# Kernel optimization log

Hardware: AMD Instinct MI355X
Metric: run time of the kernel (lower is better)

## Reference

```python
import jax, jax.numpy as jnp
import numpy as np

N = 100000   # nodes
E = 1000000  # edges
IN = 100     # input feature dim
H = 4        # heads
D = 32       # hidden per head (H*D = 128)
C = 47       # classes
EPS = 1e-5
SLOPE = 0.2  # DGL GATv2 leaky_relu negative slope


def setup_inputs() -> dict:
    key = jax.random.key(0)
    ks = jax.random.split(key, 32)
    lin = lambda k, i, o: (jax.random.normal(k, (i, o), jnp.float32) / np.float32(np.sqrt(i)))
    inp = {}
    inp['x'] = jax.random.normal(ks[0], (N, IN), jnp.float32)
    inp['src'] = jax.random.randint(ks[1], (E,), 0, N, jnp.int32)
    inp['dst'] = jnp.sort(jax.random.randint(ks[2], (E,), 0, N, jnp.int32))
    # layer 0: IN -> H*D, Linear residual (IN != H*D)
    inp['Wsrc0'] = lin(ks[3], IN, H * D); inp['bsrc0'] = jnp.zeros(H * D, jnp.float32)
    inp['Wdst0'] = lin(ks[4], IN, H * D); inp['bdst0'] = jnp.zeros(H * D, jnp.float32)
    inp['attn0'] = lin(ks[5], H, D)
    inp['Wres0'] = lin(ks[6], IN, H * D); inp['bres0'] = jnp.zeros(H * D, jnp.float32)
    # layer 1: H*D -> H*D, Identity residual (128 == 128)
    inp['Wsrc1'] = lin(ks[7], H * D, H * D); inp['bsrc1'] = jnp.zeros(H * D, jnp.float32)
    inp['Wdst1'] = lin(ks[8], H * D, H * D); inp['bdst1'] = jnp.zeros(H * D, jnp.float32)
    inp['attn1'] = lin(ks[9], H, D)
    # layer 2: H*D -> H*C, Linear residual (128 != 188)
    inp['Wsrc2'] = lin(ks[10], H * D, H * C); inp['bsrc2'] = jnp.zeros(H * C, jnp.float32)
    inp['Wdst2'] = lin(ks[11], H * D, H * C); inp['bdst2'] = jnp.zeros(H * C, jnp.float32)
    inp['attn2'] = lin(ks[12], H, C)
    inp['Wres2'] = lin(ks[13], H * D, H * C); inp['bres2'] = jnp.zeros(H * C, jnp.float32)
    # BatchNorm1d params (training-mode batch stats)
    inp['g0'] = jnp.ones(H * D, jnp.float32); inp['be0'] = jnp.zeros(H * D, jnp.float32)
    inp['g1'] = jnp.ones(H * D, jnp.float32); inp['be1'] = jnp.zeros(H * D, jnp.float32)
    return inp


def _gatv2(h, src, dst, Ws, bs, Wd, bd, attn, resval):
    """One GATv2Conv on a full block (src feats == dst feats == h)."""
    Hh, Dd = attn.shape
    fs = (h @ Ws + bs).reshape(-1, Hh, Dd)   # [N,H,D] src projection
    fd = (h @ Wd + bd).reshape(-1, Hh, Dd)   # [N,H,D] dst projection
    e = jax.nn.leaky_relu(fs[src] + fd[dst], SLOPE)         # [E,H,D]
    logits = jnp.einsum('ehd,hd->eh', e, attn)              # [E,H]
    m = jax.ops.segment_max(logits, dst, num_segments=N)    # per-dst max
    ex = jnp.exp(logits - m[dst])
    s = jax.ops.segment_sum(ex, dst, num_segments=N)
    alpha = ex / s[dst]                                      # edge softmax
    out = jax.ops.segment_sum(alpha[:, :, None] * fs[src], dst, num_segments=N)
    return out + resval                                      # [N,H,D]


def _bn(x, g, b):
    mu = x.mean(0)
    v = x.var(0)  # biased, as torch BN training mode
    return g * (x - mu) / jnp.sqrt(v + EPS) + b


def reference(x, src, dst,
              Wsrc0, bsrc0, Wdst0, bdst0, attn0, Wres0, bres0,
              Wsrc1, bsrc1, Wdst1, bdst1, attn1,
              Wsrc2, bsrc2, Wdst2, bdst2, attn2, Wres2, bres2,
              g0, be0, g1, be1):
    # layer 0: conv(+relu activation) -> flatten -> BN -> relu (dropout = eval identity)
    res0 = (x @ Wres0 + bres0).reshape(N, H, D)
    h = jax.nn.relu(_gatv2(x, src, dst, Wsrc0, bsrc0, Wdst0, bdst0, attn0, res0))
    h = jax.nn.relu(_bn(h.reshape(N, H * D), g0, be0))
    # layer 1: Identity residual
    res1 = h.reshape(N, H, D)
    h = jax.nn.relu(_gatv2(h, src, dst, Wsrc1, bsrc1, Wdst1, bdst1, attn1, res1))
    h = jax.nn.relu(_bn(h.reshape(N, H * D), g1, be1))
    # layer 2: no activation; mean over heads; log_softmax
    res2 = (h @ Wres2 + bres2).reshape(N, H, C)
    h = _gatv2(h, src, dst, Wsrc2, bsrc2, Wdst2, bdst2, attn2, res2)
    h = h.mean(1)                                # [N,C]
    return jax.nn.log_softmax(h, axis=-1)
```

## Files before the change

### kernel.cpp

```cpp
#include <hip/hip_runtime.h>
#include <hip/hip_bf16.h>

#define Nn 100000
#define Ee 1000000
#define INF_ 100
#define Hh 4
#define Dd 32
#define HD 128
#define Cc 47
#define HC 188
#define HCP 192
#define EPSV 1e-5f
#define SLOPE 0.2f

typedef __hip_bfloat16 bf16;
typedef __attribute__((ext_vector_type(8))) short short8;
typedef __attribute__((ext_vector_type(4))) float f32x4;

__device__ __forceinline__ float tof(bf16 v) { return __bfloat162float(v); }
__device__ __forceinline__ float b2f(unsigned short u) {
    return __uint_as_float((unsigned)u << 16);
}
__device__ __forceinline__ float ldb(const bf16* p) {
    return b2f(*(const unsigned short*)p);
}
__device__ __forceinline__ unsigned short f2u(float v) {
    bf16 t = __float2bfloat16(v);
    return *(unsigned short*)&t;
}

__global__ void detect_dtype(const unsigned* __restrict__ x, int* __restrict__ flag) {
    if (blockIdx.x == 0 && threadIdx.x == 0) {
        int good = 0;
        for (int i = 0; i < 256; ++i) {
            unsigned lo = x[i] & 0xFFFFu;
            float v = __uint_as_float(lo << 16);
            float a = fabsf(v);
            if (a > 1e-4f && a < 10.f) good++;
        }
        *flag = (good >= 128) ? 1 : 0;
    }
}

__device__ __forceinline__ float ld_any(const void* p, int i, int isbf) {
    return isbf ? tof(((const bf16*)p)[i]) : ((const float*)p)[i];
}

__global__ void cvt_x(const void* __restrict__ in, bf16* __restrict__ out,
                      const int* __restrict__ flag) {
    int i = blockIdx.x * blockDim.x + threadIdx.x;
    if (i >= Nn * 128) return;
    int row = i >> 7, col = i & 127;
    float v = (col < INF_) ? ld_any(in, row * INF_ + col, *flag) : 0.f;
    out[i] = __float2bfloat16(v);
}

#define NSP 15
struct CvtTab { const void* src[NSP]; int off[NSP + 1]; };

__global__ void cvt_params(CvtTab t, bf16* __restrict__ out, int total,
                           const int* __restrict__ flag) {
    int i = blockIdx.x * blockDim.x + threadIdx.x;
    if (i >= total) return;
    int isbf = *flag;
    int seg = 0;
    while (i >= t.off[seg + 1]) seg++;
    out[i] = __float2bfloat16(ld_any(t.src[seg], i - t.off[seg], isbf));
}

#define WROWS 1280
struct PrepTab { const void* src[8]; int row0[8]; int K[8]; int M[8]; int MP[8]; };

__global__ void prep_all(PrepTab t, bf16* __restrict__ wtb, const int* __restrict__ flag) {
    int i = blockIdx.x * blockDim.x + threadIdx.x;
    if (i >= WROWS * 128) return;
    int row = i >> 7, k = i & 127;
    int isbf = *flag;
    float v = 0.f;
#pragma unroll
    for (int q = 0; q < 8; ++q) {
        if (row >= t.row0[q] && row < t.row0[q] + t.MP[q]) {
            int m = row - t.row0[q];
            if (m < t.M[q] && k < t.K[q])
                v = ld_any(t.src[q], k * t.M[q] + m, isbf);
        }
    }
    wtb[i] = __float2bfloat16(v);
}

__global__ void zero_u32(unsigned* __restrict__ p, int n) {
    int i = blockIdx.x * blockDim.x + threadIdx.x;
    if (i < n) p[i] = 0u;
}

__global__ void build_ptr(const int* __restrict__ dst, int* __restrict__ ptr) {
    int n = blockIdx.x * blockDim.x + threadIdx.x;
    if (n > Nn) return;
    if (n == Nn) { ptr[Nn] = Ee; return; }
    int lo = 0, hi = Ee;
    while (lo < hi) {
        int mid = (lo + hi) >> 1;
        if (dst[mid] < n) lo = mid + 1; else hi = mid;
    }
    ptr[n] = lo;
}

template <int MP, int NOUT, int CS, bool ABN, bool PAD47, int OSTR>
__global__ __launch_bounds__(256, 4) void gemm_big(
    const bf16* __restrict__ A, const bf16* __restrict__ Wt,
    const bf16* __restrict__ b0, const bf16* __restrict__ b1,
    const bf16* __restrict__ b2,
    bf16* __restrict__ o0, bf16* __restrict__ o1, bf16* __restrict__ o2,
    int MR, const float* __restrict__ bnp) {
    __shared__ __align__(16) bf16 Al[64 * 136];
    const int row0 = blockIdx.x * 64;
    const int tid = threadIdx.x;
#pragma unroll
    for (int j = 0; j < 4; ++j) {
        int idx = tid + j * 256;
        int r = idx >> 4, kk = (idx & 15) * 8;
        int4 val = {0, 0, 0, 0};
        if (row0 + r < Nn) {
            val = *(const int4*)&A[(size_t)(row0 + r) * 128 + kk];
            if (ABN) {
                short8 av = *(short8*)&val;
                bf16 tmp[8];
#pragma unroll
                for (int u = 0; u < 8; ++u) {
                    float v = b2f((unsigned short)av[u]);
                    v = fmaxf(fmaf(v, bnp[kk + u], bnp[128 + kk + u]), 0.f);
                    tmp[u] = __float2bfloat16(v);
                }
                val = *(int4*)tmp;
            }
        }
        *(int4*)&Al[r * 136 + kk] = val;
    }
    __syncthreads();
    const int wave = tid >> 6, lane = tid & 63;
    const int n16 = lane & 15, quad = lane >> 4;
    const int colbase = blockIdx.y * (64 * CS) + wave * (16 * CS);
    f32x4 acc[4][CS];
#pragma unroll
    for (int rt = 0; rt < 4; ++rt)
#pragma unroll
        for (int c = 0; c < CS; ++c) acc[rt][c] = (f32x4){0.f, 0.f, 0.f, 0.f};
    const bf16* wb[CS];
#pragma unroll
    for (int c = 0; c < CS; ++c)
        wb[c] = Wt + (size_t)(colbase + c * 16 + n16) * 128 + quad * 8;
    const bf16* ap = Al + n16 * 136 + quad * 8;
#pragma unroll
    for (int ks = 0; ks < 4; ++ks) {
        short8 bf[CS];
#pragma unroll
        for (int c = 0; c < CS; ++c) bf[c] = *(const short8*)(wb[c] + ks * 32);
#pragma unroll
        for (int rt = 0; rt < 4; ++rt) {
            short8 af = *(const short8*)(ap + rt * 16 * 136 + ks * 32);
#pragma unroll
            for (int c = 0; c < CS; ++c)
                acc[rt][c] = __builtin_amdgcn_mfma_f32_16x16x32_bf16(af, bf[c], acc[rt][c], 0, 0, 0);
        }
    }
#pragma unroll
    for (int c = 0; c < CS; ++c) {
        int col = colbase + c * 16 + n16;
        int oi = col / MP, lc = col - oi * MP;
        if (oi >= NOUT || lc >= MR) continue;
        const bf16* bp = (oi == 0) ? b0 : (oi == 1) ? b1 : b2;
        bf16* o = (oi == 0) ? o0 : (oi == 1) ? o1 : o2;
        float bb = tof(bp[lc]);
        int st = PAD47 ? (lc + lc / 47) : lc;
#pragma unroll
        for (int rt = 0; rt < 4; ++rt) {
#pragma unroll
            for (int i = 0; i < 4; ++i) {
                int row = row0 + rt * 16 + quad * 4 + i;
                if (row < Nn)
                    o[(size_t)row * OSTR + st] = __float2bfloat16(acc[rt][c][i] + bb);
            }
        }
    }
}

template <bool RESBN>
__global__ __launch_bounds__(256) void gat_fused_128(
    const bf16* __restrict__ fs, const bf16* __restrict__ fd,
    const int* __restrict__ srcI, const int* __restrict__ ptr,
    const bf16* __restrict__ attn, const bf16* __restrict__ resb,
    const float* __restrict__ bnp, bf16* __restrict__ hout) {
    const int wave = threadIdx.x >> 6, lane = threadIdx.x & 63;
    const int d = blockIdx.x * 4 + wave;
    if (d >= Nn) return;
    const int c0 = lane * 2;
    ushort2 aq = *(const ushort2*)&attn[c0];
    float A0 = 0.6f * b2f(aq.x), B0 = 0.4f * b2f(aq.x);
    float A1 = 0.6f * b2f(aq.y), B1 = 0.4f * b2f(aq.y);
    ushort2 dq = *(const ushort2*)&fd[(size_t)d * HD + c0];
    float fd0 = b2f(dq.x), fd1 = b2f(dq.y);
    float l = 0.f, O0 = 0.f, O1 = 0.f;
    int e = ptr[d];
    const int e1 = ptr[d + 1];
    for (; e + 3 < e1; e += 4) {
        int sA = srcI[e], sB = srcI[e + 1], sC = srcI[e + 2], sD = srcI[e + 3];
        ushort2 qA = *(const ushort2*)&fs[(size_t)sA * HD + c0];
        ushort2 qB = *(const ushort2*)&fs[(size_t)sB * HD + c0];
        ushort2 qC = *(const ushort2*)&fs[(size_t)sC * HD + c0];
        ushort2 qD = *(const ushort2*)&fs[(size_t)sD * HD + c0];
        float fA0 = b2f(qA.x), fA1 = b2f(qA.y);
        float fB0 = b2f(qB.x), fB1 = b2f(qB.y);
        float fC0 = b2f(qC.x), fC1 = b2f(qC.y);
        float fD0 = b2f(qD.x), fD1 = b2f(qD.y);
        float xA0 = fA0 + fd0, xA1 = fA1 + fd1;
        float xB0 = fB0 + fd0, xB1 = fB1 + fd1;
        float xC0 = fC0 + fd0, xC1 = fC1 + fd1;
        float xD0 = fD0 + fd0, xD1 = fD1 + fd1;
        float pA = fmaf(xA0, A0, fmaf(fabsf(xA0), B0, fmaf(xA1, A1, fabsf(xA1) * B1)));
        float pB = fmaf(xB0, A0, fmaf(fabsf(xB0), B0, fmaf(xB1, A1, fabsf(xB1) * B1)));
        float pC = fmaf(xC0, A0, fmaf(fabsf(xC0), B0, fmaf(xC1, A1, fabsf(xC1) * B1)));
        float pD = fmaf(xD0, A0, fmaf(fabsf(xD0), B0, fmaf(xD1, A1, fabsf(xD1) * B1)));
        pA += __shfl_xor(pA, 1); pB += __shfl_xor(pB, 1);
        pC += __shfl_xor(pC, 1); pD += __shfl_xor(pD, 1);
        pA += __shfl_xor(pA, 2); pB += __shfl_xor(pB, 2);
        pC += __shfl_xor(pC, 2); pD += __shfl_xor(pD, 2);
        pA += __shfl_xor(pA, 4); pB += __shfl_xor(pB, 4);
        pC += __shfl_xor(pC, 4); pD += __shfl_xor(pD, 4);
        pA += __shfl_xor(pA, 8); pB += __shfl_xor(pB, 8);
        pC += __shfl_xor(pC, 8); pD += __shfl_xor(pD, 8);
        float eA = __expf(pA), eB = __expf(pB), eC = __expf(pC), eD = __expf(pD);
        l += (eA + eB) + (eC + eD);
        O0 = fmaf(eA, fA0, O0); O0 = fmaf(eB, fB0, O0);
        O0 = fmaf(eC, fC0, O0); O0 = fmaf(eD, fD0, O0);
        O1 = fmaf(eA, fA1, O1); O1 = fmaf(eB, fB1, O1);
        O1 = fmaf(eC, fC1, O1); O1 = fmaf(eD, fD1, O1);
    }
    for (; e < e1; ++e) {
        int s = srcI[e];
        ushort2 fq = *(const ushort2*)&fs[(size_t)s * HD + c0];
        float f0 = b2f(fq.x), f1 = b2f(fq.y);
        float x0 = f0 + fd0, x1 = f1 + fd1;
        float p = fmaf(x0, A0, fmaf(fabsf(x0), B0, fmaf(x1, A1, fabsf(x1) * B1)));
        p += __shfl_xor(p, 1); p += __shfl_xor(p, 2);
        p += __shfl_xor(p, 4); p += __shfl_xor(p, 8);
        float pe = __expf(p);
        l += pe;
        O0 = fmaf(pe, f0, O0);
        O1 = fmaf(pe, f1, O1);
    }
    float inv = l > 0.f ? 1.f / l : 0.f;
    ushort2 rq = *(const ushort2*)&resb[(size_t)d * HD + c0];
    float r0 = b2f(rq.x), r1 = b2f(rq.y);
    if (RESBN) {
        r0 = fmaxf(fmaf(r0, bnp[c0], bnp[HD + c0]), 0.f);
        r1 = fmaxf(fmaf(r1, bnp[c0 + 1], bnp[HD + c0 + 1]), 0.f);
    }
    float v0 = fmaxf(fmaf(O0, inv, r0), 0.f);
    float v1 = fmaxf(fmaf(O1, inv, r1), 0.f);
    ushort2 ov; ov.x = f2u(v0); ov.y = f2u(v1);
    *(ushort2*)&hout[(size_t)d * HD + c0] = ov;
}

__global__ __launch_bounds__(256) void gat_fused_188(
    const bf16* __restrict__ fs, const bf16* __restrict__ fd,
    const int* __restrict__ srcI, const int* __restrict__ ptr,
    const bf16* __restrict__ attn, const bf16* __restrict__ rs,
    void* __restrict__ out, const int* __restrict__ flag) {
    const int wave = threadIdx.x >> 6, lane = threadIdx.x & 63;
    const int d = blockIdx.x * 4 + wave;
    if (d >= Nn) return;
    const int h = lane >> 4, j = lane & 15;
    const int c0 = h * 48 + j;
    const int ca = h * Cc + j;
    const bool has2 = (j < 15);
    float a0 = ldb(&attn[ca]);
    float a1 = ldb(&attn[ca + 16]);
    float a2 = has2 ? ldb(&attn[ca + 32]) : 0.f;
    float A0 = 0.6f * a0, B0 = 0.4f * a0;
    float A1 = 0.6f * a1, B1 = 0.4f * a1;
    float A2 = 0.6f * a2, B2 = 0.4f * a2;
    const bf16* fdr = fd + (size_t)d * HCP;
    float fd0 = ldb(&fdr[c0]);
    float fd1 = ldb(&fdr[c0 + 16]);
    float fd2 = ldb(&fdr[c0 + 32]);
    float l = 0.f, O0 = 0.f, O1 = 0.f, O2 = 0.f;
    int e = ptr[d];
    const int e1 = ptr[d + 1];
    for (; e + 3 < e1; e += 4) {
        int sA = srcI[e], sB = srcI[e + 1], sC = srcI[e + 2], sD = srcI[e + 3];
        const bf16* frA = fs + (size_t)sA * HCP;
        const bf16* frB = fs + (size_t)sB * HCP;
        const bf16* frC = fs + (size_t)sC * HCP;
        const bf16* frD = fs + (size_t)sD * HCP;
        float fA0 = ldb(&frA[c0]), fA1 = ldb(&frA[c0 + 16]), fA2 = ldb(&frA[c0 + 32]);
        float fB0 = ldb(&frB[c0]), fB1 = ldb(&frB[c0 + 16]), fB2 = ldb(&frB[c0 + 32]);
        float fC0 = ldb(&frC[c0]), fC1 = ldb(&frC[c0 + 16]), fC2 = ldb(&frC[c0 + 32]);
        float fD0 = ldb(&frD[c0]), fD1 = ldb(&frD[c0 + 16]), fD2 = ldb(&frD[c0 + 32]);
        float xA0 = fA0 + fd0, xA1 = fA1 + fd1, xA2 = fA2 + fd2;
        float xB0 = fB0 + fd0, xB1 = fB1 + fd1, xB2 = fB2 + fd2;
        float xC0 = fC0 + fd0, xC1 = fC1 + fd1, xC2 = fC2 + fd2;
        float xD0 = fD0 + fd0, xD1 = fD1 + fd1, xD2 = fD2 + fd2;
        float pA = fmaf(xA0, A0, fmaf(fabsf(xA0), B0, fmaf(xA1, A1, fmaf(fabsf(xA1), B1,
                   fmaf(xA2, A2, fabsf(xA2) * B2)))));
        float pB = fmaf(xB0, A0, fmaf(fabsf(xB0), B0, fmaf(xB1, A1, fmaf(fabsf(xB1), B1,
                   fmaf(xB2, A2, fabsf(xB2) * B2)))));
        float pC = fmaf(xC0, A0, fmaf(fabsf(xC0), B0, fmaf(xC1, A1, fmaf(fabsf(xC1), B1,
                   fmaf(xC2, A2, fabsf(xC2) * B2)))));
        float pD = fmaf(xD0, A0, fmaf(fabsf(xD0), B0, fmaf(xD1, A1, fmaf(fabsf(xD1), B1,
                   fmaf(xD2, A2, fabsf(xD2) * B2)))));
        pA += __shfl_xor(pA, 1); pB += __shfl_xor(pB, 1);
        pC += __shfl_xor(pC, 1); pD += __shfl_xor(pD, 1);
        pA += __shfl_xor(pA, 2); pB += __shfl_xor(pB, 2);
        pC += __shfl_xor(pC, 2); pD += __shfl_xor(pD, 2);
        pA += __shfl_xor(pA, 4); pB += __shfl_xor(pB, 4);
        pC += __shfl_xor(pC, 4); pD += __shfl_xor(pD, 4);
        pA += __shfl_xor(pA, 8); pB += __shfl_xor(pB, 8);
        pC += __shfl_xor(pC, 8); pD += __shfl_xor(pD, 8);
        float eA = __expf(pA), eB = __expf(pB), eC = __expf(pC), eD = __expf(pD);
        l += (eA + eB) + (eC + eD);
        O0 = fmaf(eA, fA0, O0); O0 = fmaf(eB, fB0, O0);
        O0 = fmaf(eC, fC0, O0); O0 = fmaf(eD, fD0, O0);
        O1 = fmaf(eA, fA1, O1); O1 = fmaf(eB, fB1, O1);
        O1 = fmaf(eC, fC1, O1); O1 = fmaf(eD, fD1, O1);
        O2 = fmaf(eA, fA2, O2); O2 = fmaf(eB, fB2, O2);
        O2 = fmaf(eC, fC2, O2); O2 = fmaf(eD, fD2, O2);
    }
    for (; e < e1; ++e) {
        int s = srcI[e];
        const bf16* fr = fs + (size_t)s * HCP;
        float f0 = ldb(&fr[c0]);
        float f1 = ldb(&fr[c0 + 16]);
        float f2 = ldb(&fr[c0 + 32]);
        float x0 = f0 + fd0, x1 = f1 + fd1, x2 = f2 + fd2;
        float p = fmaf(x0, A0, fmaf(fabsf(x0), B0, fmaf(x1, A1, fmaf(fabsf(x1), B1,
                  fmaf(x2, A2, fabsf(x2) * B2)))));
        p += __shfl_xor(p, 1); p += __shfl_xor(p, 2);
        p += __shfl_xor(p, 4); p += __shfl_xor(p, 8);
        float pe = __expf(p);
        l += pe;
        O0 = fmaf(pe, f0, O0);
        O1 = fmaf(pe, f1, O1);
        O2 = fmaf(pe, f2, O2);
    }
    float inv = l > 0.f ? 1.f / l : 0.f;
    const bf16* rr = rs + (size_t)d * HCP;
    float v0 = fmaf(O0, inv, ldb(&rr[c0]));
    float v1 = fmaf(O1, inv, ldb(&rr[c0 + 16]));
    float v2 = has2 ? fmaf(O2, inv, ldb(&rr[c0 + 32])) : 0.f;
    v0 += __shfl_xor(v0, 16); v0 += __shfl_xor(v0, 32); v0 *= 0.25f;
    v1 += __shfl_xor(v1, 16); v1 += __shfl_xor(v1, 32); v1 *= 0.25f;
    v2 += __shfl_xor(v2, 16); v2 += __shfl_xor(v2, 32); v2 *= 0.25f;
    float mx = fmaxf(v0, v1);
    if (has2) mx = fmaxf(mx, v2);
    mx = fmaxf(mx, __shfl_xor(mx, 1)); mx = fmaxf(mx, __shfl_xor(mx, 2));
    mx = fmaxf(mx, __shfl_xor(mx, 4)); mx = fmaxf(mx, __shfl_xor(mx, 8));
    float sm = __expf(v0 - mx) + __expf(v1 - mx) + (has2 ? __expf(v2 - mx) : 0.f);
    sm += __shfl_xor(sm, 1); sm += __shfl_xor(sm, 2);
    sm += __shfl_xor(sm, 4); sm += __shfl_xor(sm, 8);
    if (h == 0) {
        float ls = mx + logf(sm);
        if (*flag) {
            bf16* o = (bf16*)out + (size_t)d * Cc;
            o[j] = __float2bfloat16(v0 - ls);
            o[j + 16] = __float2bfloat16(v1 - ls);
            if (has2) o[j + 32] = __float2bfloat16(v2 - ls);
        } else {
            float* o = (float*)out + (size_t)d * Cc;
            o[j] = v0 - ls;
            o[j + 16] = v1 - ls;
            if (has2) o[j + 32] = v2 - ls;
        }
    }
}

__global__ void col_stats(const bf16* __restrict__ in, float* __restrict__ sums) {
    int c = threadIdx.x;
    int r0 = blockIdx.x * 256;
    int r1 = r0 + 256; if (r1 > Nn) r1 = Nn;
    float s = 0.f, s2 = 0.f;
    for (int r = r0; r < r1; ++r) {
        float v = ldb(&in[(size_t)r * HD + c]);
        s += v; s2 += v * v;
    }
    atomicAdd(&sums[c], s);
    atomicAdd(&sums[HD + c], s2);
}

__global__ void bn_finalize(const float* __restrict__ sums, const bf16* __restrict__ g,
                            const bf16* __restrict__ be, float* __restrict__ ss) {
    int c = threadIdx.x;
    float mu = sums[c] * (1.f / Nn);
    float var = sums[HD + c] * (1.f / Nn) - mu * mu;
    float sc = tof(g[c]) * rsqrtf(var + EPSV);
    ss[c] = sc;
    ss[HD + c] = tof(be[c]) - mu * sc;
}

extern "C" void kernel_launch(void* const* d_in, const int* in_sizes, int n_in,
                              void* d_out, int out_size, void* d_ws, size_t ws_size,
                              hipStream_t stream) {
    (void)in_sizes; (void)n_in; (void)out_size; (void)ws_size;
    const void* x = d_in[0];
    const int* src = (const int*)d_in[1];
    const int* dst = (const int*)d_in[2];

    char* ws = (char*)d_ws;
    size_t off = 0;
    auto alloc = [&](size_t bytes) {
        void* p = ws + off;
        off += (bytes + 255) & ~(size_t)255;
        return p;
    };
    bf16* xb = (bf16*)alloc((size_t)Nn * 128 * 2);
    bf16* rb = (bf16*)alloc((size_t)Nn * HD * 2);
    bf16* rs = xb;
    bf16* fs = (bf16*)alloc((size_t)Nn * HCP * 2);
    bf16* fd = (bf16*)alloc((size_t)Nn * HCP * 2);
    bf16* hbA = (bf16*)alloc((size_t)Nn * HD * 2);
    bf16* hbB = (bf16*)alloc((size_t)Nn * HD * 2);
    int* ptr = (int*)alloc((Nn + 1) * 4);
    bf16* wtb = (bf16*)alloc((size_t)WROWS * 128 * 2);
    float* bns = (float*)alloc(2 * HD * 4);
    float* bnss0 = (float*)alloc(2 * HD * 4);
    float* bnss1 = (float*)alloc(2 * HD * 4);
    bf16* pb = (bf16*)alloc(4096 * 2);
    int* flag = (int*)alloc(256);

    static const int spIdx[NSP] = {4, 6, 7, 9, 11, 13, 14, 16, 18, 19, 21, 22, 23, 24, 25};
    static const int spSz[NSP]  = {HD, HD, HD, HD, HD, HD, HD, HC, HC, HC, HC, HD, HD, HD, HD};
    CvtTab tab;
    int tot = 0;
    for (int i = 0; i < NSP; ++i) { tab.src[i] = d_in[spIdx[i]]; tab.off[i] = tot; tot += spSz[i]; }
    tab.off[NSP] = tot;
    const bf16 *bsrc0 = pb + tab.off[0], *bdst0 = pb + tab.off[1], *attn0 = pb + tab.off[2],
               *bres0 = pb + tab.off[3], *bsrc1 = pb + tab.off[4], *bdst1 = pb + tab.off[5],
               *attn1 = pb + tab.off[6], *bsrc2 = pb + tab.off[7], *bdst2 = pb + tab.off[8],
               *attn2 = pb + tab.off[9], *bres2 = pb + tab.off[10],
               *g0 = pb + tab.off[11], *be0 = pb + tab.off[12],
               *g1 = pb + tab.off[13], *be1 = pb + tab.off[14];

    PrepTab pt;
    static const int wIdx[8] = {3, 5, 8, 10, 12, 15, 17, 20};
    static const int wK[8]   = {INF_, INF_, INF_, HD, HD, HD, HD, HD};
    static const int wM[8]   = {HD, HD, HD, HD, HD, HC, HC, HC};
    static const int wMP[8]  = {128, 128, 128, 128, 128, 192, 192, 192};
    static const int wR0[8]  = {0, 128, 256, 384, 512, 640, 832, 1024};
    for (int i = 0; i < 8; ++i) {
        pt.src[i] = d_in[wIdx[i]]; pt.row0[i] = wR0[i];
        pt.K[i] = wK[i]; pt.M[i] = wM[i]; pt.MP[i] = wMP[i];
    }

    detect_dtype<<<1, 64, 0, stream>>>((const unsigned*)x, flag);
    cvt_x<<<(Nn * 128 + 255) / 256, 256, 0, stream>>>(x, xb, flag);
    cvt_params<<<(tot + 255) / 256, 256, 0, stream>>>(tab, pb, tot, flag);
    prep_all<<<(WROWS * 128 + 255) / 256, 256, 0, stream>>>(pt, wtb, flag);
    build_ptr<<<(Nn + 256) / 256, 256, 0, stream>>>(dst, ptr);

    const int fusedGrid = (Nn + 3) / 4;
    const int statsGrid = (Nn + 255) / 256;
    const int rowBlk = (Nn + 63) / 64;

    gemm_big<128, 3, 3, false, false, HD><<<dim3(rowBlk, 2), 256, 0, stream>>>(
        xb, wtb, bsrc0, bdst0, bres0, fs, fd, rb, HD, nullptr);
    gat_fused_128<false><<<fusedGrid, 256, 0, stream>>>(fs, fd, src, ptr, attn0,
                                                        rb, nullptr, hbA);
    zero_u32<<<1, 256, 0, stream>>>((unsigned*)bns, 2 * HD);
    col_stats<<<statsGrid, 128, 0, stream>>>(hbA, bns);
    bn_finalize<<<1, HD, 0, stream>>>(bns, g0, be0, bnss0);

    gemm_big<128, 2, 2, true, false, HD><<<dim3(rowBlk, 2), 256, 0, stream>>>(
        hbA, wtb + (size_t)384 * 128, bsrc1, bdst1, nullptr, fs, fd, nullptr, HD, bnss0);
    gat_fused_128<true><<<fusedGrid, 256, 0, stream>>>(fs, fd, src, ptr, attn1,
                                                       hbA, bnss0, hbB);
    zero_u32<<<1, 256, 0, stream>>>((unsigned*)bns, 2 * HD);
    col_stats<<<statsGrid, 128, 0, stream>>>(hbB, bns);
    bn_finalize<<<1, HD, 0, stream>>>(bns, g1, be1, bnss1);

    gemm_big<192, 3, 3, true, true, HCP><<<dim3(rowBlk, 3), 256, 0, stream>>>(
        hbB, wtb + (size_t)640 * 128, bsrc2, bdst2, bres2, fs, fd, rs, HC, bnss1);
    gat_fused_188<<<fusedGrid, 256, 0, stream>>>(fs, fd, src, ptr, attn2, rs,
                                                 d_out, flag);
}
```

Before: 681.2 us.

## Degree-sort destinations, prescale src offsets, use DPP reductions and exp2

Adds preprocessing kernels that sort destination nodes by in-degree into a permutation so each wave's work is more uniform. Source indices are precomputed as byte offsets to remove multiply and 64-bit address math in the gather loops. The shfl_xor head reductions become DPP row operations, and exp is replaced by hardware exp2 with attention weights prescaled by log2(e). This adds several small setup kernels and 8 MB of extra index traffic, and the permuted order may scatter the output writes.

Result: slower. 1.324 ms (+94.3%).

```diff
diff --git a/kernel.cpp b/kernel.cpp
--- a/kernel.cpp
+++ b/kernel.cpp
@@ -29,6 +29,31 @@
     return *(unsigned short*)&t;
 }
 
+template <int C>
+__device__ __forceinline__ float dppadd(float v) {
+    int m = __builtin_amdgcn_update_dpp(0, __float_as_int(v), C, 0xF, 0xF, false);
+    return v + __int_as_float(m);
+}
+template <int C>
+__device__ __forceinline__ float dppmax(float v) {
+    int m = __builtin_amdgcn_update_dpp(0, __float_as_int(v), C, 0xF, 0xF, false);
+    return fmaxf(v, __int_as_float(m));
+}
+__device__ __forceinline__ float sum16(float p) {
+    p = dppadd<0xB1>(p);
+    p = dppadd<0x4E>(p);
+    p = dppadd<0x124>(p);
+    p = dppadd<0x128>(p);
+    return p;
+}
+__device__ __forceinline__ float max16(float p) {
+    p = dppmax<0xB1>(p); p = dppmax<0x4E>(p);
+    p = dppmax<0x124>(p); p = dppmax<0x128>(p);
+    return p;
+}
+
+#define L2E 1.4426950408889634f
+
 __global__ void detect_dtype(const unsigned* __restrict__ x, int* __restrict__ flag) {
     if (blockIdx.x == 0 && threadIdx.x == 0) {
         int good = 0;
@@ -105,6 +130,36 @@
     ptr[n] = lo;
 }
 
+__global__ void src_scale(const int* __restrict__ src, unsigned* __restrict__ w384,
+                          unsigned* __restrict__ w256) {
+    int i = blockIdx.x * blockDim.x + threadIdx.x;
+    if (i >= Ee) return;
+    unsigned s = (unsigned)src[i];
+    w384[i] = s * 384u;
+    w256[i] = s << 8;
+}
+
+__global__ void deg_hist(const int* __restrict__ ptr, int* __restrict__ hist) {
+    int n = blockIdx.x * blockDim.x + threadIdx.x;
+    if (n >= Nn) return;
+    int dg = ptr[n + 1] - ptr[n]; if (dg > 255) dg = 255;
+    atomicAdd(&hist[dg], 1);
+}
+__global__ void deg_scan(const int* __restrict__ hist, int* __restrict__ base) {
+    int t = threadIdx.x;
+    int acc = 0;
+    for (int b = t + 1; b < 256; ++b) acc += hist[b];
+    base[t] = acc;
+}
+__global__ void deg_scatter(const int* __restrict__ ptr, int* __restrict__ base,
+                            int* __restrict__ perm) {
+    int n = blockIdx.x * blockDim.x + threadIdx.x;
+    if (n >= Nn) return;
+    int dg = ptr[n + 1] - ptr[n]; if (dg > 255) dg = 255;
+    int pos = atomicAdd(&base[dg], 1);
+    perm[pos] = n;
+}
+
 template <int MP, int NOUT, int CS, bool ABN, bool PAD47, int OSTR>
 __global__ __launch_bounds__(256, 4) void gemm_big(
     const bf16* __restrict__ A, const bf16* __restrict__ Wt,
@@ -187,27 +242,33 @@
 template <bool RESBN>
 __global__ __launch_bounds__(256) void gat_fused_128(
     const bf16* __restrict__ fs, const bf16* __restrict__ fd,
-    const int* __restrict__ srcI, const int* __restrict__ ptr,
+    const unsigned* __restrict__ srcW, const int* __restrict__ ptr,
+    const int* __restrict__ perm,
     const bf16* __restrict__ attn, const bf16* __restrict__ resb,
     const float* __restrict__ bnp, bf16* __restrict__ hout) {
     const int wave = threadIdx.x >> 6, lane = threadIdx.x & 63;
-    const int d = blockIdx.x * 4 + wave;
-    if (d >= Nn) return;
+    const int di = blockIdx.x * 4 + wave;
+    if (di >= Nn) return;
+    const int d = perm[di];
     const int c0 = lane * 2;
+    const unsigned c0b = (unsigned)c0 * 2u;
     ushort2 aq = *(const ushort2*)&attn[c0];
-    float A0 = 0.6f * b2f(aq.x), B0 = 0.4f * b2f(aq.x);
-    float A1 = 0.6f * b2f(aq.y), B1 = 0.4f * b2f(aq.y);
+    float a0 = b2f(aq.x) * L2E, a1 = b2f(aq.y) * L2E;
+    float A0 = 0.6f * a0, B0 = 0.4f * a0;
+    float A1 = 0.6f * a1, B1 = 0.4f * a1;
     ushort2 dq = *(const ushort2*)&fd[(size_t)d * HD + c0];
     float fd0 = b2f(dq.x), fd1 = b2f(dq.y);
+    const char* fsb = (const char*)fs;
     float l = 0.f, O0 = 0.f, O1 = 0.f;
     int e = ptr[d];
     const int e1 = ptr[d + 1];
     for (; e + 3 < e1; e += 4) {
-        int sA = srcI[e], sB = srcI[e + 1], sC = srcI[e + 2], sD = srcI[e + 3];
-        ushort2 qA = *(const ushort2*)&fs[(size_t)sA * HD + c0];
-        ushort2 qB = *(const ushort2*)&fs[(size_t)sB * HD + c0];
-        ushort2 qC = *(const ushort2*)&fs[(size_t)sC * HD + c0];
-        ushort2 qD = *(const ushort2*)&fs[(size_t)sD * HD + c0];
+        unsigned vA = srcW[e] + c0b, vB = srcW[e + 1] + c0b;
+        unsigned vC = srcW[e + 2] + c0b, vD = srcW[e + 3] + c0b;
+        ushort2 qA = *(const ushort2*)(fsb + vA);
+        ushort2 qB = *(const ushort2*)(fsb + vB);
+        ushort2 qC = *(const ushort2*)(fsb + vC);
+        ushort2 qD = *(const ushort2*)(fsb + vD);
         float fA0 = b2f(qA.x), fA1 = b2f(qA.y);
         float fB0 = b2f(qB.x), fB1 = b2f(qB.y);
         float fC0 = b2f(qC.x), fC1 = b2f(qC.y);
@@ -220,15 +281,9 @@
         float pB = fmaf(xB0, A0, fmaf(fabsf(xB0), B0, fmaf(xB1, A1, fabsf(xB1) * B1)));
         float pC = fmaf(xC0, A0, fmaf(fabsf(xC0), B0, fmaf(xC1, A1, fabsf(xC1) * B1)));
         float pD = fmaf(xD0, A0, fmaf(fabsf(xD0), B0, fmaf(xD1, A1, fabsf(xD1) * B1)));
-        pA += __shfl_xor(pA, 1); pB += __shfl_xor(pB, 1);
-        pC += __shfl_xor(pC, 1); pD += __shfl_xor(pD, 1);
-        pA += __shfl_xor(pA, 2); pB += __shfl_xor(pB, 2);
-        pC += __shfl_xor(pC, 2); pD += __shfl_xor(pD, 2);
-        pA += __shfl_xor(pA, 4); pB += __shfl_xor(pB, 4);
-        pC += __shfl_xor(pC, 4); pD += __shfl_xor(pD, 4);
-        pA += __shfl_xor(pA, 8); pB += __shfl_xor(pB, 8);
-        pC += __shfl_xor(pC, 8); pD += __shfl_xor(pD, 8);
-        float eA = __expf(pA), eB = __expf(pB), eC = __expf(pC), eD = __expf(pD);
+        pA = sum16(pA); pB = sum16(pB); pC = sum16(pC); pD = sum16(pD);
+        float eA = __builtin_amdgcn_exp2f(pA), eB = __builtin_amdgcn_exp2f(pB);
+        float eC = __builtin_amdgcn_exp2f(pC), eD = __builtin_amdgcn_exp2f(pD);
         l += (eA + eB) + (eC + eD);
         O0 = fmaf(eA, fA0, O0); O0 = fmaf(eB, fB0, O0);
         O0 = fmaf(eC, fC0, O0); O0 = fmaf(eD, fD0, O0);
@@ -236,14 +291,13 @@
         O1 = fmaf(eC, fC1, O1); O1 = fmaf(eD, fD1, O1);
     }
     for (; e < e1; ++e) {
-        int s = srcI[e];
-        ushort2 fq = *(const ushort2*)&fs[(size_t)s * HD + c0];
+        unsigned v = srcW[e] + c0b;
+        ushort2 fq = *(const ushort2*)(fsb + v);
         float f0 = b2f(fq.x), f1 = b2f(fq.y);
         float x0 = f0 + fd0, x1 = f1 + fd1;
         float p = fmaf(x0, A0, fmaf(fabsf(x0), B0, fmaf(x1, A1, fabsf(x1) * B1)));
-        p += __shfl_xor(p, 1); p += __shfl_xor(p, 2);
-        p += __shfl_xor(p, 4); p += __shfl_xor(p, 8);
-        float pe = __expf(p);
+        p = sum16(p);
+        float pe = __builtin_amdgcn_exp2f(p);
         l += pe;
         O0 = fmaf(pe, f0, O0);
         O1 = fmaf(pe, f1, O1);
@@ -263,19 +317,22 @@
 
 __global__ __launch_bounds__(256) void gat_fused_188(
     const bf16* __restrict__ fs, const bf16* __restrict__ fd,
-    const int* __restrict__ srcI, const int* __restrict__ ptr,
+    const unsigned* __restrict__ srcW, const int* __restrict__ ptr,
+    const int* __restrict__ perm,
     const bf16* __restrict__ attn, const bf16* __restrict__ rs,
     void* __restrict__ out, const int* __restrict__ flag) {
     const int wave = threadIdx.x >> 6, lane = threadIdx.x & 63;
-    const int d = blockIdx.x * 4 + wave;
-    if (d >= Nn) return;
+    const int di = blockIdx.x * 4 + wave;
+    if (di >= Nn) return;
+    const int d = perm[di];
     const int h = lane >> 4, j = lane & 15;
     const int c0 = h * 48 + j;
+    const unsigned c0b = (unsigned)c0 * 2u;
     const int ca = h * Cc + j;
     const bool has2 = (j < 15);
-    float a0 = ldb(&attn[ca]);
-    float a1 = ldb(&attn[ca + 16]);
-    float a2 = has2 ? ldb(&attn[ca + 32]) : 0.f;
+    float a0 = ldb(&attn[ca]) * L2E;
+    float a1 = ldb(&attn[ca + 16]) * L2E;
+    float a2 = has2 ? ldb(&attn[ca + 32]) * L2E : 0.f;
     float A0 = 0.6f * a0, B0 = 0.4f * a0;
     float A1 = 0.6f * a1, B1 = 0.4f * a1;
     float A2 = 0.6f * a2, B2 = 0.4f * a2;
@@ -283,19 +340,25 @@
     float fd0 = ldb(&fdr[c0]);
     float fd1 = ldb(&fdr[c0 + 16]);
     float fd2 = ldb(&fdr[c0 + 32]);
+    const char* fsb = (const char*)fs;
     float l = 0.f, O0 = 0.f, O1 = 0.f, O2 = 0.f;
     int e = ptr[d];
     const int e1 = ptr[d + 1];
     for (; e + 3 < e1; e += 4) {
-        int sA = srcI[e], sB = srcI[e + 1], sC = srcI[e + 2], sD = srcI[e + 3];
-        const bf16* frA = fs + (size_t)sA * HCP;
-        const bf16* frB = fs + (size_t)sB * HCP;
-        const bf16* frC = fs + (size_t)sC * HCP;
-        const bf16* frD = fs + (size_t)sD * HCP;
-        float fA0 = ldb(&frA[c0]), fA1 = ldb(&frA[c0 + 16]), fA2 = ldb(&frA[c0 + 32]);
-        float fB0 = ldb(&frB[c0]), fB1 = ldb(&frB[c0 + 16]), fB2 = ldb(&frB[c0 + 32]);
-        float fC0 = ldb(&frC[c0]), fC1 = ldb(&frC[c0 + 16]), fC2 = ldb(&frC[c0 + 32]);
-        float fD0 = ldb(&frD[c0]), fD1 = ldb(&frD[c0 + 16]), fD2 = ldb(&frD[c0 + 32]);
+        unsigned vA = srcW[e] + c0b, vB = srcW[e + 1] + c0b;
+        unsigned vC = srcW[e + 2] + c0b, vD = srcW[e + 3] + c0b;
+        float fA0 = b2f(*(const unsigned short*)(fsb + vA));
+        float fA1 = b2f(*(const unsigned short*)(fsb + vA + 32));
+        float fA2 = b2f(*(const unsigned short*)(fsb + vA + 64));
+        float fB0 = b2f(*(const unsigned short*)(fsb + vB));
+        float fB1 = b2f(*(const unsigned short*)(fsb + vB + 32));
+        float fB2 = b2f(*(const unsigned short*)(fsb + vB + 64));
+        float fC0 = b2f(*(const unsigned short*)(fsb + vC));
+        float fC1 = b2f(*(const unsigned short*)(fsb + vC + 32));
+        float fC2 = b2f(*(const unsigned short*)(fsb + vC + 64));
+        float fD0 = b2f(*(const unsigned short*)(fsb + vD));
+        float fD1 = b2f(*(const unsigned short*)(fsb + vD + 32));
+        float fD2 = b2f(*(const unsigned short*)(fsb + vD + 64));
         float xA0 = fA0 + fd0, xA1 = fA1 + fd1, xA2 = fA2 + fd2;
         float xB0 = fB0 + fd0, xB1 = fB1 + fd1, xB2 = fB2 + fd2;
         float xC0 = fC0 + fd0, xC1 = fC1 + fd1, xC2 = fC2 + fd2;
@@ -308,15 +371,9 @@
                    fmaf(xC2, A2, fabsf(xC2) * B2)))));
         float pD = fmaf(xD0, A0, fmaf(fabsf(xD0), B0, fmaf(xD1, A1, fmaf(fabsf(xD1), B1,
                    fmaf(xD2, A2, fabsf(xD2) * B2)))));
-        pA += __shfl_xor(pA, 1); pB += __shfl_xor(pB, 1);
-        pC += __shfl_xor(pC, 1); pD += __shfl_xor(pD, 1);
-        pA += __shfl_xor(pA, 2); pB += __shfl_xor(pB, 2);
-        pC += __shfl_xor(pC, 2); pD += __shfl_xor(pD, 2);
-        pA += __shfl_xor(pA, 4); pB += __shfl_xor(pB, 4);
-        pC += __shfl_xor(pC, 4); pD += __shfl_xor(pD, 4);
-        pA += __shfl_xor(pA, 8); pB += __shfl_xor(pB, 8);
-        pC += __shfl_xor(pC, 8); pD += __shfl_xor(pD, 8);
-        float eA = __expf(pA), eB = __expf(pB), eC = __expf(pC), eD = __expf(pD);
+        pA = sum16(pA); pB = sum16(pB); pC = sum16(pC); pD = sum16(pD);
+        float eA = __builtin_amdgcn_exp2f(pA), eB = __builtin_amdgcn_exp2f(pB);
+        float eC = __builtin_amdgcn_exp2f(pC), eD = __builtin_amdgcn_exp2f(pD);
         l += (eA + eB) + (eC + eD);
         O0 = fmaf(eA, fA0, O0); O0 = fmaf(eB, fB0, O0);
         O0 = fmaf(eC, fC0, O0); O0 = fmaf(eD, fD0, O0);
@@ -326,17 +383,15 @@
         O2 = fmaf(eC, fC2, O2); O2 = fmaf(eD, fD2, O2);
     }
     for (; e < e1; ++e) {
-        int s = srcI[e];
-        const bf16* fr = fs + (size_t)s * HCP;
-        float f0 = ldb(&fr[c0]);
-        float f1 = ldb(&fr[c0 + 16]);
-        float f2 = ldb(&fr[c0 + 32]);
+        unsigned v = srcW[e] + c0b;
+        float f0 = b2f(*(const unsigned short*)(fsb + v));
+        float f1 = b2f(*(const unsigned short*)(fsb + v + 32));
+        float f2 = b2f(*(const unsigned short*)(fsb + v + 64));
         float x0 = f0 + fd0, x1 = f1 + fd1, x2 = f2 + fd2;
         float p = fmaf(x0, A0, fmaf(fabsf(x0), B0, fmaf(x1, A1, fmaf(fabsf(x1), B1,
                   fmaf(x2, A2, fabsf(x2) * B2)))));
-        p += __shfl_xor(p, 1); p += __shfl_xor(p, 2);
-        p += __shfl_xor(p, 4); p += __shfl_xor(p, 8);
-        float pe = __expf(p);
+        p = sum16(p);
+        float pe = __builtin_amdgcn_exp2f(p);
         l += pe;
         O0 = fmaf(pe, f0, O0);
         O1 = fmaf(pe, f1, O1);
@@ -352,11 +407,9 @@
     v2 += __shfl_xor(v2, 16); v2 += __shfl_xor(v2, 32); v2 *= 0.25f;
     float mx = fmaxf(v0, v1);
     if (has2) mx = fmaxf(mx, v2);
-    mx = fmaxf(mx, __shfl_xor(mx, 1)); mx = fmaxf(mx, __shfl_xor(mx, 2));
-    mx = fmaxf(mx, __shfl_xor(mx, 4)); mx = fmaxf(mx, __shfl_xor(mx, 8));
+    mx = max16(mx);
     float sm = __expf(v0 - mx) + __expf(v1 - mx) + (has2 ? __expf(v2 - mx) : 0.f);
-    sm += __shfl_xor(sm, 1); sm += __shfl_xor(sm, 2);
-    sm += __shfl_xor(sm, 4); sm += __shfl_xor(sm, 8);
+    sm = sum16(sm);
     if (h == 0) {
         float ls = mx + logf(sm);
         if (*flag) {
@@ -425,6 +478,11 @@
     float* bnss1 = (float*)alloc(2 * HD * 4);
     bf16* pb = (bf16*)alloc(4096 * 2);
     int* flag = (int*)alloc(256);
+    unsigned* w384 = (unsigned*)alloc((size_t)Ee * 4);
+    unsigned* w256 = (unsigned*)alloc((size_t)Ee * 4);
+    int* hist = (int*)alloc(256 * 4);
+    int* bbase = (int*)alloc(256 * 4);
+    int* perm = (int*)alloc((size_t)Nn * 4);
 
     static const int spIdx[NSP] = {4, 6, 7, 9, 11, 13, 14, 16, 18, 19, 21, 22, 23, 24, 25};
     static const int spSz[NSP]  = {HD, HD, HD, HD, HD, HD, HD, HC, HC, HC, HC, HD, HD, HD, HD};
@@ -455,6 +513,11 @@
     cvt_params<<<(tot + 255) / 256, 256, 0, stream>>>(tab, pb, tot, flag);
     prep_all<<<(WROWS * 128 + 255) / 256, 256, 0, stream>>>(pt, wtb, flag);
     build_ptr<<<(Nn + 256) / 256, 256, 0, stream>>>(dst, ptr);
+    src_scale<<<(Ee + 255) / 256, 256, 0, stream>>>(src, w384, w256);
+    zero_u32<<<1, 256, 0, stream>>>((unsigned*)hist, 256);
+    deg_hist<<<(Nn + 255) / 256, 256, 0, stream>>>(ptr, hist);
+    deg_scan<<<1, 256, 0, stream>>>(hist, bbase);
+    deg_scatter<<<(Nn + 255) / 256, 256, 0, stream>>>(ptr, bbase, perm);
 
     const int fusedGrid = (Nn + 3) / 4;
     const int statsGrid = (Nn + 255) / 256;
@@ -462,22 +525,22 @@
 
     gemm_big<128, 3, 3, false, false, HD><<<dim3(rowBlk, 2), 256, 0, stream>>>(
         xb, wtb, bsrc0, bdst0, bres0, fs, fd, rb, HD, nullptr);
-    gat_fused_128<false><<<fusedGrid, 256, 0, stream>>>(fs, fd, src, ptr, attn0,
-                                                        rb, nullptr, hbA);
+    gat_fused_128<false><<<fusedGrid, 256, 0, stream>>>(fs, fd, w256, ptr, perm,
+                                                        attn0, rb, nullptr, hbA);
     zero_u32<<<1, 256, 0, stream>>>((unsigned*)bns, 2 * HD);
     col_stats<<<statsGrid, 128, 0, stream>>>(hbA, bns);
     bn_finalize<<<1, HD, 0, stream>>>(bns, g0, be0, bnss0);
 
     gemm_big<128, 2, 2, true, false, HD><<<dim3(rowBlk, 2), 256, 0, stream>>>(
         hbA, wtb + (size_t)384 * 128, bsrc1, bdst1, nullptr, fs, fd, nullptr, HD, bnss0);
-    gat_fused_128<true><<<fusedGrid, 256, 0, stream>>>(fs, fd, src, ptr, attn1,
-                                                       hbA, bnss0, hbB);
+    gat_fused_128<true><<<fusedGrid, 256, 0, stream>>>(fs, fd, w256, ptr, perm,
+                                                       attn1, hbA, bnss0, hbB);
     zero_u32<<<1, 256, 0, stream>>>((unsigned*)bns, 2 * HD);
     col_stats<<<statsGrid, 128, 0, stream>>>(hbB, bns);
     bn_finalize<<<1, HD, 0, stream>>>(bns, g1, be1, bnss1);
 
     gemm_big<192, 3, 3, true, true, HCP><<<dim3(rowBlk, 3), 256, 0, stream>>>(
         hbB, wtb + (size_t)640 * 128, bsrc2, bdst2, bres2, fs, fd, rs, HC, bnss1);
-    gat_fused_188<<<fusedGrid, 256, 0, stream>>>(fs, fd, src, ptr, attn2, rs,
+    gat_fused_188<<<fusedGrid, 256, 0, stream>>>(fs, fd, w384, ptr, perm, attn2, rs,
                                                  d_out, flag);
 }
```
